# Kernel tuning notes

Hardware: AMD Instinct MI355X
Metric: run time of the kernel (lower is better)

## Reference

```python
import jax, jax.numpy as jnp
import numpy as np

EPS = 1e-12  # matches torch F.normalize default eps (clamp_min)
B, C, N = 32, 512, 4096
K_CLUSTERS, G_CLUSTERS = 64, 8
T_CLUSTERS = K_CLUSTERS + G_CLUSTERS  # 72
H_ATTN = T_CLUSTERS // 4  # 18


def _l2norm(v, axis):
    return v / jnp.maximum(jnp.linalg.norm(v, axis=axis, keepdims=True), EPS)


def setup_inputs() -> dict:
    key = jax.random.key(0)
    ks = jax.random.split(key, 6)
    x = jax.random.normal(ks[0], (B, C, N), dtype=jnp.float32)
    centroids = jax.random.normal(ks[1], (T_CLUSTERS, C), dtype=jnp.float32) * 0.01
    # 1x1 Conv2d(C -> T) == dense [T, C] weight + bias
    conv_w = jax.random.normal(ks[2], (T_CLUSTERS, C), dtype=jnp.float32) / np.sqrt(C).astype(np.float32)
    conv_b = jnp.zeros((T_CLUSTERS,), dtype=jnp.float32)
    ghost_weights = jnp.ones((G_CLUSTERS,), dtype=jnp.float32) * 0.1
    w1 = jax.random.normal(ks[3], (H_ATTN, T_CLUSTERS), dtype=jnp.float32) / np.sqrt(T_CLUSTERS).astype(np.float32)
    b1 = jnp.zeros((H_ATTN,), dtype=jnp.float32)
    w2 = jax.random.normal(ks[4], (T_CLUSTERS, H_ATTN), dtype=jnp.float32) / np.sqrt(H_ATTN).astype(np.float32)
    b2 = jnp.zeros((T_CLUSTERS,), dtype=jnp.float32)
    return {"x": x, "centroids": centroids, "conv_w": conv_w, "conv_b": conv_b,
            "ghost_weights": ghost_weights, "w1": w1, "b1": b1, "w2": w2, "b2": b2}


def reference(x, centroids, conv_w, conv_b, ghost_weights, w1, b1, w2, b2):
    # x: [B, C, N] -> L2 normalize over channel dim
    xn = _l2norm(x, axis=1)
    # 1x1 conv -> soft assignment logits [B, T, N], softmax over clusters
    logits = jnp.einsum('kc,bcn->bkn', conv_w, xn) + conv_b[None, :, None]
    assign = jax.nn.softmax(logits, axis=1)
    # residual aggregation, algebraically fused:
    # vlad[b,k,c] = sum_n a[b,k,n]*x[b,c,n] - centroid[k,c]*sum_n a[b,k,n]
    agg = jnp.einsum('bkn,bcn->bkc', assign, xn)
    mass = assign.sum(axis=-1)  # [B, T]
    vlad = agg - centroids[None, :, :] * mass[:, :, None]
    # ghost cluster down-weighting
    gw = jax.nn.softmax(ghost_weights)
    vlad = vlad.at[:, K_CLUSTERS:, :].multiply(gw[None, :, None])
    # attention over clusters: mean over C -> MLP -> softmax over clusters
    scores = vlad.mean(axis=-1)  # [B, T]
    h = jax.nn.relu(scores @ w1.T + b1)
    attn = jax.nn.softmax(h @ w2.T + b2, axis=1)
    vlad = vlad * attn[:, :, None]
    # intra-cluster L2 norm, drop ghosts, flatten, global L2 norm
    vlad = _l2norm(vlad, axis=2)
    vlad = vlad[:, :K_CLUSTERS, :].reshape(vlad.shape[0], -1)
    return _l2norm(vlad, axis=1)
```

## Files before the change

kernel.cpp:

```cpp
#include <hip/hip_runtime.h>
#include <hip/hip_bf16.h>

#define B_ 32
#define C_ 512
#define N_ 4096
#define T_ 72
#define K_ 64
#define KP 80
#define EPSF 1e-12f

typedef unsigned short u16;
typedef unsigned int u32;
typedef __attribute__((ext_vector_type(8))) short bf16x8;
typedef __attribute__((ext_vector_type(4))) float f32x4;

__device__ __forceinline__ u16 f2bf(float v) {
    __hip_bfloat16 h = __float2bfloat16(v);
    return *reinterpret_cast<u16*>(&h);
}

__global__ __launch_bounds__(256) void k_prep(
    const float* __restrict__ conv_w, const float* __restrict__ conv_b,
    u16* __restrict__ Wp, float* __restrict__ bp)
{
    const int idx = blockIdx.x * 256 + threadIdx.x;
    if (idx < KP * C_) {
        const int k = idx >> 9, c = idx & (C_ - 1);
        Wp[idx] = f2bf(k < T_ ? conv_w[k * C_ + c] : 0.f);
    } else if (idx < KP * C_ + KP) {
        const int j = idx - KP * C_;
        bp[j] = (j < T_) ? conv_b[j] : -1e30f;
    }
}

#define ANW 256
__global__ __launch_bounds__(256, 2) void k_assign(
    const float* __restrict__ x, const u16* __restrict__ Wp,
    const float* __restrict__ bp, u16* __restrict__ assignp,
    float* __restrict__ mass)
{
    __shared__ u16   xs[ANW * 32];
    __shared__ float red[4][ANW];
    __shared__ float inv_sh[ANW];

    const int t = threadIdx.x;
    const int b = blockIdx.y;
    const int n0 = blockIdx.x * ANW;
    const int lane = t & 63, w = t >> 6;
    const int q = lane >> 4, nl = lane & 15;

    const float* xb = x + (size_t)b * C_ * N_ + n0 + 4 * lane;

    f32x4 acc[4][5];
    #pragma unroll
    for (int nt = 0; nt < 4; ++nt)
        #pragma unroll
        for (int mt = 0; mt < 5; ++mt) acc[nt][mt] = (f32x4)0.f;
    float ss[4] = {0.f, 0.f, 0.f, 0.f};

    float4 v[8];
    bf16x8 af[5];
    #pragma unroll
    for (int i = 0; i < 8; ++i)
        v[i] = *(const float4*)(xb + (size_t)(w * 8 + i) * N_);
    #pragma unroll
    for (int mt = 0; mt < 5; ++mt)
        af[mt] = *(const bf16x8*)(Wp + (size_t)(mt * 16 + nl) * C_ + q * 8);

#define VJ(i) (j == 0 ? v[i].x : j == 1 ? v[i].y : j == 2 ? v[i].z : v[i].w)

    #pragma unroll 1
    for (int ch = 0; ch < 16; ++ch) {
        #pragma unroll
        for (int j = 0; j < 4; ++j) {
            const float f0 = VJ(0), f1 = VJ(1), f2 = VJ(2), f3 = VJ(3);
            const float f4 = VJ(4), f5 = VJ(5), f6 = VJ(6), f7 = VJ(7);
            ss[j] = fmaf(f0, f0, ss[j]); ss[j] = fmaf(f1, f1, ss[j]);
            ss[j] = fmaf(f2, f2, ss[j]); ss[j] = fmaf(f3, f3, ss[j]);
            ss[j] = fmaf(f4, f4, ss[j]); ss[j] = fmaf(f5, f5, ss[j]);
            ss[j] = fmaf(f6, f6, ss[j]); ss[j] = fmaf(f7, f7, ss[j]);
            uint4 pk;
            pk.x = (u32)f2bf(f0) | ((u32)f2bf(f1) << 16);
            pk.y = (u32)f2bf(f2) | ((u32)f2bf(f3) << 16);
            pk.z = (u32)f2bf(f4) | ((u32)f2bf(f5) << 16);
            pk.w = (u32)f2bf(f6) | ((u32)f2bf(f7) << 16);
            const int n = 4 * lane + j;
            const int slot = (w + ((lane >> 1) & 3)) & 3;
            *(uint4*)&xs[n * 32 + slot * 8] = pk;
        }
        __syncthreads();
        if (ch < 15) {
            #pragma unroll
            for (int i = 0; i < 8; ++i)
                v[i] = *(const float4*)(xb + (size_t)((ch + 1) * 32 + w * 8 + i) * N_);
        }
        __builtin_amdgcn_sched_barrier(0);
        #pragma unroll
        for (int nt = 0; nt < 4; ++nt) {
            const int n = (4 * w + nt) * 16 + nl;
            const int slot = (q + ((n >> 3) & 3)) & 3;
            const bf16x8 bfr = *(const bf16x8*)&xs[n * 32 + slot * 8];
            #pragma unroll
            for (int mt = 0; mt < 5; ++mt)
                acc[nt][mt] = __builtin_amdgcn_mfma_f32_16x16x32_bf16(af[mt], bfr, acc[nt][mt], 0, 0, 0);
        }
        if (ch < 15) {
            #pragma unroll
            for (int mt = 0; mt < 5; ++mt)
                af[mt] = *(const bf16x8*)(Wp + (size_t)(mt * 16 + nl) * C_ + (ch + 1) * 32 + q * 8);
        }
        __syncthreads();
    }
#undef VJ

    *(float4*)&red[w][4 * lane] = make_float4(ss[0], ss[1], ss[2], ss[3]);
    __syncthreads();
    {
        const float s = red[0][t] + red[1][t] + red[2][t] + red[3][t];
        inv_sh[t] = 1.0f / fmaxf(sqrtf(s), EPSF);
    }
    __syncthreads();

    float bpv[5][4];
    #pragma unroll
    for (int mt = 0; mt < 5; ++mt)
        #pragma unroll
        for (int r = 0; r < 4; ++r) bpv[mt][r] = bp[mt * 16 + q * 4 + r];

    #pragma unroll
    for (int nt = 0; nt < 4; ++nt) {
        const int n_loc = (4 * w + nt) * 16 + nl;
        const float invn = inv_sh[n_loc];
        const int nglob = n0 + n_loc;

        float lg[5][4];
        #pragma unroll
        for (int mt = 0; mt < 5; ++mt)
            #pragma unroll
            for (int r = 0; r < 4; ++r)
                lg[mt][r] = acc[nt][mt][r] * invn + bpv[mt][r];

        float mx = -1e30f;
        #pragma unroll
        for (int mt = 0; mt < 5; ++mt)
            #pragma unroll
            for (int r = 0; r < 4; ++r) mx = fmaxf(mx, lg[mt][r]);
        mx = fmaxf(mx, __shfl_xor(mx, 16, 64));
        mx = fmaxf(mx, __shfl_xor(mx, 32, 64));

        float s = 0.f;
        #pragma unroll
        for (int mt = 0; mt < 5; ++mt)
            #pragma unroll
            for (int r = 0; r < 4; ++r) {
                lg[mt][r] = __expf(lg[mt][r] - mx);
                s += lg[mt][r];
            }
        s += __shfl_xor(s, 16, 64);
        s += __shfl_xor(s, 32, 64);
        const float rs = 1.0f / s;

        #pragma unroll
        for (int mt = 0; mt < 4; ++mt)
            #pragma unroll
            for (int r = 0; r < 4; ++r) {
                const float a = lg[mt][r] * rs;
                float msum = a;
                msum += __shfl_xor(msum, 1, 64);
                msum += __shfl_xor(msum, 2, 64);
                msum += __shfl_xor(msum, 4, 64);
                msum += __shfl_xor(msum, 8, 64);
                const int k = mt * 16 + q * 4 + r;
                if (nl == 0) atomicAdd(&mass[b * K_ + k], msum);
                assignp[((size_t)b * K_ + k) * N_ + nglob] = f2bf(a * invn);
            }
    }
}

#define GBK 64
#define NCH 8
__global__ __launch_bounds__(256) void k_agg(
    const float* __restrict__ x, const u16* __restrict__ assignp,
    float* __restrict__ out)
{
    __shared__ u16 Bt[4][16][72];

    const int t  = threadIdx.x;
    const int b  = blockIdx.z;
    const int nc0 = blockIdx.y * (N_ / NCH);
    const int c0  = blockIdx.x * 64;

    const int lane = t & 63, w = t >> 6;
    const int q = lane >> 4, nl = lane & 15;
    const int nq16 = lane & 15, cj = lane >> 4;

    f32x4 acc[4];
    #pragma unroll
    for (int mt = 0; mt < 4; ++mt) acc[mt] = (f32x4)0.f;

    const u16*   ab = assignp + (size_t)b * K_ * N_ + (size_t)nl * N_ + q * 8;
    const float* xb = x + ((size_t)b * C_ + c0 + 16 * w) * N_ + 4 * nq16;

    float4 vb[4];
    #pragma unroll
    for (int p = 0; p < 4; ++p)
        vb[p] = *(const float4*)(xb + (size_t)(4 * p + cj) * N_ + nc0);

    #pragma unroll 1
    for (int n0 = nc0; n0 < nc0 + N_ / NCH; n0 += GBK) {
        #pragma unroll
        for (int p = 0; p < 4; ++p) {
            const float4 v = vb[p];
            uint2 pk;
            pk.x = (u32)f2bf(v.x) | ((u32)f2bf(v.y) << 16);
            pk.y = (u32)f2bf(v.z) | ((u32)f2bf(v.w) << 16);
            *(uint2*)&Bt[w][4 * p + cj][4 * nq16] = pk;
        }
        if (n0 + GBK < nc0 + N_ / NCH) {
            #pragma unroll
            for (int p = 0; p < 4; ++p)
                vb[p] = *(const float4*)(xb + (size_t)(4 * p + cj) * N_ + n0 + GBK);
        }
        #pragma unroll
        for (int kk = 0; kk < 2; ++kk) {
            const bf16x8 bfr = *(const bf16x8*)&Bt[w][nl][kk * 32 + q * 8];
            #pragma unroll
            for (int mt = 0; mt < 4; ++mt) {
                const bf16x8 af = *(const bf16x8*)(ab + (size_t)(mt * 16) * N_ + n0 + kk * 32);
                acc[mt] = __builtin_amdgcn_mfma_f32_16x16x32_bf16(af, bfr, acc[mt], 0, 0, 0);
            }
        }
    }

    float* ob = out + (size_t)b * K_ * C_;
    const int c = c0 + 16 * w + nl;
    #pragma unroll
    for (int mt = 0; mt < 4; ++mt)
        #pragma unroll
        for (int r = 0; r < 4; ++r)
            atomicAdd(&ob[(size_t)(mt * 16 + q * 4 + r) * C_ + c], acc[mt][r]);
}

__device__ __forceinline__ float block_reduce_sum_256(float v) {
    #pragma unroll
    for (int o = 32; o > 0; o >>= 1) v += __shfl_down(v, o, 64);
    __shared__ float wsh[4];
    const int lane = threadIdx.x & 63, wid = threadIdx.x >> 6;
    if (lane == 0) wsh[wid] = v;
    __syncthreads();
    float r = 0.f;
    if (threadIdx.x == 0) r = wsh[0] + wsh[1] + wsh[2] + wsh[3];
    return r;
}

__global__ __launch_bounds__(256) void k_rnorm(
    const float* __restrict__ agg, const float* __restrict__ centroids,
    const float* __restrict__ mass, float* __restrict__ rnorm,
    float* __restrict__ gsum)
{
    const int k = blockIdx.x, b = blockIdx.y;
    const float mk = mass[b * K_ + k];
    const float* p  = agg + ((size_t)b * K_ + k) * C_;
    const float* cb = centroids + k * C_;
    float s = 0.f;
    #pragma unroll 2
    for (int i = threadIdx.x; i < C_; i += 256) {
        const float v = fmaf(-cb[i], mk, p[i]);
        s = fmaf(v, v, s);
    }
    const float ss = block_reduce_sum_256(s);
    if (threadIdx.x == 0) {
        const float rn = fmaxf(sqrtf(ss), EPSF);
        rnorm[b * K_ + k] = rn;
        atomicAdd(gsum + b, ss / (rn * rn));
    }
}

__global__ __launch_bounds__(256) void k_final(
    float* __restrict__ out, const float* __restrict__ centroids,
    const float* __restrict__ mass, const float* __restrict__ rnorm,
    const float* __restrict__ gsum)
{
    const size_t i4 = ((size_t)blockIdx.x * 256 + threadIdx.x) * 4;
    const int b = (int)(i4 >> 15);
    const int k = (int)((i4 >> 9) & 63);
    const int c = (int)(i4 & 511);
    const float gn = fmaxf(sqrtf(gsum[b]), EPSF);
    const float sc = 1.0f / (rnorm[b * K_ + k] * gn);
    const float mk = mass[b * K_ + k];
    float4 v  = *(const float4*)(out + i4);
    const float4 cv = *(const float4*)(centroids + k * C_ + c);
    v.x = fmaf(-cv.x, mk, v.x) * sc;
    v.y = fmaf(-cv.y, mk, v.y) * sc;
    v.z = fmaf(-cv.z, mk, v.z) * sc;
    v.w = fmaf(-cv.w, mk, v.w) * sc;
    *(float4*)(out + i4) = v;
}

extern "C" void kernel_launch(void* const* d_in, const int* in_sizes, int n_in,
                              void* d_out, int out_size, void* d_ws, size_t ws_size,
                              hipStream_t stream) {
    const float* x         = (const float*)d_in[0];
    const float* centroids = (const float*)d_in[1];
    const float* conv_w    = (const float*)d_in[2];
    const float* conv_b    = (const float*)d_in[3];

    float* out = (float*)d_out;
    char*  ws  = (char*)d_ws;

    u16*   assignp = (u16*)ws;
    u16*   Wp      = (u16*)(ws + 16777216);
    float* bpad    = (float*)(ws + 16777216 + 81920);
    float* mass    = (float*)(ws + 16777216 + 81920 + 320);
    float* rnorm   = mass + B_ * K_;
    float* gsum    = rnorm + B_ * K_;

    hipMemsetAsync(mass, 0, B_ * K_ * sizeof(float), stream);
    hipMemsetAsync(gsum, 0, B_ * sizeof(float), stream);
    hipMemsetAsync(out, 0, (size_t)out_size * sizeof(float), stream);

    k_prep<<<dim3((KP * C_ + KP + 255) / 256), 256, 0, stream>>>(conv_w, conv_b, Wp, bpad);
    k_assign<<<dim3(N_ / ANW, B_), 256, 0, stream>>>(x, Wp, bpad, assignp, mass);
    k_agg<<<dim3(C_ / 64, NCH, B_), 256, 0, stream>>>(x, assignp, out);
    k_rnorm<<<dim3(K_, B_), 256, 0, stream>>>(out, centroids, mass, rnorm, gsum);
    k_final<<<(out_size / 4 + 255) / 256, 256, 0, stream>>>(out, centroids, mass, rnorm, gsum);
}
```

Measured before the change: 507.6 us.

## Restructure k_agg staging to wide coalesced row loads with larger N tiles

The aggregation kernel now has each wave load 16 full channel rows of 256 contiguous N elements (1 KB per row per wave), instead of the earlier scattered 64-element tiles. It stages them as bf16 into a block-shared LDS tile of 64x264 and runs 8 MFMA k-steps per tile. The N-chunk per block doubles from 512 to 1024, so the grid shrinks and fewer atomics hit the output. The intent is better global-load coalescing and fewer outer iterations. In exchange it drops the register prefetch double-buffering, adds two block barriers per tile, and uses more LDS per block.

After: 509.8 us. About the same (+0.4%).

```diff
diff --git a/kernel.cpp b/kernel.cpp
--- a/kernel.cpp
+++ b/kernel.cpp
@@ -177,59 +177,51 @@
     }
 }
 
-#define GBK 64
-#define NCH 8
+#define AGW 1024
+#define AGS 256
+#define AGP 264
 __global__ __launch_bounds__(256) void k_agg(
     const float* __restrict__ x, const u16* __restrict__ assignp,
     float* __restrict__ out)
 {
-    __shared__ u16 Bt[4][16][72];
-
-    const int t  = threadIdx.x;
-    const int b  = blockIdx.z;
-    const int nc0 = blockIdx.y * (N_ / NCH);
-    const int c0  = blockIdx.x * 64;
-
+    __shared__ u16 Bt[K_][AGP];
+
+    const int t = threadIdx.x, b = blockIdx.z;
+    const int nc0 = blockIdx.y * AGW;
+    const int c0 = blockIdx.x * 64;
     const int lane = t & 63, w = t >> 6;
     const int q = lane >> 4, nl = lane & 15;
-    const int nq16 = lane & 15, cj = lane >> 4;
 
     f32x4 acc[4];
     #pragma unroll
     for (int mt = 0; mt < 4; ++mt) acc[mt] = (f32x4)0.f;
 
     const u16*   ab = assignp + (size_t)b * K_ * N_ + (size_t)nl * N_ + q * 8;
-    const float* xb = x + ((size_t)b * C_ + c0 + 16 * w) * N_ + 4 * nq16;
-
-    float4 vb[4];
-    #pragma unroll
-    for (int p = 0; p < 4; ++p)
-        vb[p] = *(const float4*)(xb + (size_t)(4 * p + cj) * N_ + nc0);
+    const float* xb = x + ((size_t)b * C_ + c0) * N_;
 
     #pragma unroll 1
-    for (int n0 = nc0; n0 < nc0 + N_ / NCH; n0 += GBK) {
-        #pragma unroll
-        for (int p = 0; p < 4; ++p) {
-            const float4 v = vb[p];
+    for (int p = 0; p < AGW / AGS; ++p) {
+        const int n0 = nc0 + p * AGS;
+        #pragma unroll
+        for (int i = 0; i < 16; ++i) {
+            const int cr = 16 * w + i;
+            const float4 vv = *(const float4*)(xb + (size_t)cr * N_ + n0 + 4 * lane);
             uint2 pk;
-            pk.x = (u32)f2bf(v.x) | ((u32)f2bf(v.y) << 16);
-            pk.y = (u32)f2bf(v.z) | ((u32)f2bf(v.w) << 16);
-            *(uint2*)&Bt[w][4 * p + cj][4 * nq16] = pk;
-        }
-        if (n0 + GBK < nc0 + N_ / NCH) {
-            #pragma unroll
-            for (int p = 0; p < 4; ++p)
-                vb[p] = *(const float4*)(xb + (size_t)(4 * p + cj) * N_ + n0 + GBK);
-        }
-        #pragma unroll
-        for (int kk = 0; kk < 2; ++kk) {
-            const bf16x8 bfr = *(const bf16x8*)&Bt[w][nl][kk * 32 + q * 8];
+            pk.x = (u32)f2bf(vv.x) | ((u32)f2bf(vv.y) << 16);
+            pk.y = (u32)f2bf(vv.z) | ((u32)f2bf(vv.w) << 16);
+            *(uint2*)&Bt[cr][4 * lane] = pk;
+        }
+        __syncthreads();
+        #pragma unroll
+        for (int ks = 0; ks < 8; ++ks) {
+            const bf16x8 bfr = *(const bf16x8*)&Bt[16 * w + nl][ks * 32 + q * 8];
             #pragma unroll
             for (int mt = 0; mt < 4; ++mt) {
-                const bf16x8 af = *(const bf16x8*)(ab + (size_t)(mt * 16) * N_ + n0 + kk * 32);
-                acc[mt] = __builtin_amdgcn_mfma_f32_16x16x32_bf16(af, bfr, acc[mt], 0, 0, 0);
+                const bf16x8 afv = *(const bf16x8*)(ab + (size_t)(mt * 16) * N_ + n0 + ks * 32);
+                acc[mt] = __builtin_amdgcn_mfma_f32_16x16x32_bf16(afv, bfr, acc[mt], 0, 0, 0);
             }
         }
+        __syncthreads();
     }
 
     float* ob = out + (size_t)b * K_ * C_;
@@ -321,7 +313,7 @@
 
     k_prep<<<dim3((KP * C_ + KP + 255) / 256), 256, 0, stream>>>(conv_w, conv_b, Wp, bpad);
     k_assign<<<dim3(N_ / ANW, B_), 256, 0, stream>>>(x, Wp, bpad, assignp, mass);
-    k_agg<<<dim3(C_ / 64, NCH, B_), 256, 0, stream>>>(x, assignp, out);
+    k_agg<<<dim3(C_ / 64, N_ / AGW, B_), 256, 0, stream>>>(x, assignp, out);
     k_rnorm<<<dim3(K_, B_), 256, 0, stream>>>(out, centroids, mass, rnorm, gsum);
     k_final<<<(out_size / 4 + 255) / 256, 256, 0, stream>>>(out, centroids, mass, rnorm, gsum);
 }
```
